# Kernel tuning notes

Measured on AMD Instinct MI355X. Metric: run time of the kernel, lower is better.

## Reference

```python
import jax, jax.numpy as jnp
import numpy as np

B, L, D = 32, 300, 256          # batch, seq (fixed 300 in module), emb_size
N = B * L                       # hypergraph nodes
NI, E, NNZ, U = 100000, 4000, 100000, 38312
LAYERS, HEADS, AH = 2, 4, 4     # conv layers, conv heads, fusing-attn heads
DU = D // 2                     # user embedding dim
DF = D + DU                     # fused dim (emb + emb//2)


def _pe_table():
    # pe[0] row is zeros (module indexes pe[0..L-1] where row 0 of buffer is zero)
    pos = jnp.arange(L, dtype=jnp.float32)[:, None]
    div = jnp.exp(jnp.arange(0, D, 2, dtype=jnp.float32) * (-np.log(10000.0) / D))
    pe = jnp.zeros((L + 1, D), jnp.float32)
    pe = pe.at[1:, 0::2].set(jnp.sin(pos * div))
    pe = pe.at[1:, 1::2].set(jnp.cos(pos * div))
    return pe[:L]  # [L, D]


def _hconv(x, W, b, node_idx, edge_idx):
    # Multi-head hypergraph conv: D^{-1} H B^{-1} H^T X Theta, heads concat back to D
    xt = (x @ W).reshape(N, HEADS, D // HEADS)
    ones = jnp.ones((NNZ,), x.dtype)
    deg_e = jnp.clip(jax.ops.segment_sum(ones, edge_idx, num_segments=E), 1.0)
    deg_n = jnp.clip(jax.ops.segment_sum(ones, node_idx, num_segments=N), 1.0)
    e = jax.ops.segment_sum(xt[node_idx], edge_idx, num_segments=E) / deg_e[:, None, None]
    o = jax.ops.segment_sum(e[edge_idx], node_idx, num_segments=N) / deg_n[:, None, None]
    return o.reshape(N, D) + b


def setup_inputs() -> dict:
    key = jax.random.key(0)
    ks = iter(jax.random.split(key, 40))
    s = 1.0 / 16.0  # stdv = 1/sqrt(emb_size) per reset_parameters
    u = lambda shape: jax.random.uniform(next(ks), shape, jnp.float32, -s, s)
    return {
        "input": jax.random.normal(next(ks), (B,), jnp.float32),
        "label": jax.random.normal(next(ks), (B,), jnp.float32),
        "text_table": jax.random.normal(next(ks), (NI, 384), jnp.float32) * 0.02,
        "img_table": jax.random.normal(next(ks), (NI, 2048), jnp.float32) * 0.02,
        "W1": u((384, D)), "b1": u((D,)),
        "W2": u((2048, D)), "b2": u((D,)),
        "user_table": u((U, DU)),
        "Wt": u((LAYERS, D, D)), "bt": u((LAYERS, D)),
        "Wi": u((LAYERS, D, D)), "bi": u((LAYERS, D)),
        "Wq": u((DF, DF)), "Wk": u((DF, DF)), "Wv": u((DF, DF)), "Wo": u((DF, DF)),
        "W3": u((2 * DF, DF)), "b3": u((DF,)),
        "Wd": u((DF, DF)), "bd": u((DF,)),
        "W4": u((DF, 1)), "b4": u((1,)),
        "related_items": jax.random.randint(next(ks), (N,), 0, NI),
        "uid": jax.random.randint(next(ks), (B,), 0, U),
        "hg_idx": jnp.stack([jax.random.randint(next(ks), (NNZ,), 0, N),
                             jax.random.randint(next(ks), (NNZ,), 0, E)]),
    }


def reference(input, label, text_table, img_table, W1, b1, W2, b2, user_table,
              Wt, bt, Wi, bi, Wq, Wk, Wv, Wo, W3, b3, Wd, bd, W4, b4,
              related_items, uid, hg_idx):
    ue = user_table[uid]                                    # [B, DU]
    pe = 0.002 * _pe_table()                                # added twice at *0.001 each
    te = (text_table[related_items] @ W1 + b1).reshape(B, L, D) + pe[None]
    ie = (img_table[related_items] @ W2 + b2).reshape(B, L, D) + pe[None]
    tg = te.reshape(N, D)
    ig = ie.reshape(N, D)
    node_idx, edge_idx = hg_idx[0], hg_idx[1]
    for l in range(LAYERS):  # fixed small layer count
        tg_new = _hconv(tg, Wt[l], bt[l], node_idx, edge_idx)
        ig = _hconv(ig, Wi[l], bi[l], node_idx, edge_idx)
        tg = tg_new
    text_user = jnp.concatenate([tg.reshape(B, L, D)[:, 0], ue], 1)  # [B, DF]
    img_user = jnp.concatenate([ig.reshape(B, L, D)[:, 0], ue], 1)   # [B, DF]
    fused = jnp.concatenate([text_user, img_user], -1) @ W3 + b3     # [B, DF]
    q = fused[:, None, :]                                   # [B, 1, DF]
    kv = jnp.stack([text_user, img_user], 1)                # [B, 2, DF]
    dh = DF // AH
    sp = lambda x: x.reshape(B, -1, AH, dh).transpose(0, 2, 1, 3)
    Qh, Kh, Vh = sp(q @ Wq), sp(kv @ Wk), sp(kv @ Wv)
    att = jax.nn.softmax(jnp.einsum('bhqd,bhkd->bhqk', Qh, Kh) / jnp.sqrt(jnp.float32(dh)), -1)
    o = jnp.einsum('bhqk,bhkd->bhqd', att, Vh).transpose(0, 2, 1, 3).reshape(B, 1, DF) @ Wo + q
    out = jax.nn.relu(o[:, 0, :] @ Wd + bd)                 # dense + ReLU
    return out @ W4 + b4                                    # [B, 1]
```

## Files before the change

kernel.cpp:

```cpp
#include <hip/hip_runtime.h>

typedef unsigned short u16;
typedef unsigned int u32;
typedef __bf16 bf16x8 __attribute__((ext_vector_type(8)));
typedef float f32x4 __attribute__((ext_vector_type(4)));

constexpr int Bn = 32, Ln = 300, Dn = 256;
constexpr int Nn = Bn * Ln;
constexpr int En = 4000, NNZn = 100000;
constexpr int DUn = 128, DFn = 384;
constexpr int PK = 512;
constexpr long NPl = (long)Nn * PK;
constexpr long EPl = (long)En * PK;
constexpr int PMAX = 1536;

constexpr int SEG_WPROD = 0;
constexpr int SEG_GIMG = SEG_WPROD + 512;
constexpr int SEG_W2T  = SEG_GIMG + 9600;
constexpr int SEG_GTXT = SEG_W2T + 2048;
constexpr int SEG_W1T  = SEG_GTXT + 2400;
constexpr int SEG_PE   = SEG_W1T + 384;
constexpr int SEG_CNT  = SEG_PE + 300;
constexpr int SEG_END  = SEG_CNT + 391;

__device__ __forceinline__ u16 f2bf(float f) {
    union { float f; u32 u; } x{f};
    u32 u = x.u;
    u32 r = (u + 0x7FFFu + ((u >> 16) & 1u)) >> 16;
    return (u16)r;
}
__device__ __forceinline__ float bf2f(u16 s) {
    union { u32 u; float f; } x{(u32)s << 16};
    return x.f;
}

__global__ __launch_bounds__(256) void prep_all(
    float* __restrict__ pe_tab,
    const float* __restrict__ W1, u16* __restrict__ W1t,
    const float* __restrict__ W2, u16* __restrict__ W2t,
    const float* __restrict__ Wt, const float* __restrict__ bt,
    const float* __restrict__ Wi, const float* __restrict__ bi,
    u16* __restrict__ W12t, float* __restrict__ bias12, float* __restrict__ bias2w,
    const int* __restrict__ node_idx, const int* __restrict__ edge_idx,
    int* __restrict__ cnt_e, int* __restrict__ cnt_n,
    const float* __restrict__ text_table, const float* __restrict__ img_table,
    const int* __restrict__ rel, u16* __restrict__ Atx, u16* __restrict__ Aim) {
    int bid = blockIdx.x;
    int t = threadIdx.x;
    if (bid < SEG_GIMG) {
        int idx = bid * 256 + t;
        int m = idx >> 16;
        int k = (idx >> 8) & 255;
        int n = idx & 255;
        const float* W0 = m ? Wi : Wt;
        const float* Wl1 = W0 + 65536;
        const float* b0 = m ? bi : bt;
        float acc = 0.f;
        for (int j = 0; j < 256; j++) acc += W0[k * 256 + j] * Wl1[j * 256 + n];
        W12t[((size_t)m << 16) + k * 256 + n] = f2bf(acc);
        if (k == 0) {
            float ba = 0.f;
            for (int j = 0; j < 256; j++) ba += b0[j] * Wl1[j * 256 + n];
            bias12[m * 256 + n] = ba + b0[256 + n];
            bias2w[m * 256 + n] = b0[256 + n];
        }
        return;
    }
    if (bid < SEG_W2T) {
        int r = bid - SEG_GIMG;
        const float4* s4 = (const float4*)(img_table + (size_t)rel[r] * 2048);
        u16* drow = Aim + (size_t)r * 2048;
#pragma unroll
        for (int i = 0; i < 2; i++) {
            int e = i * 256 + t;
            float4 v = s4[e];
            u16 o[4] = {f2bf(v.x), f2bf(v.y), f2bf(v.z), f2bf(v.w)};
            *(uint2*)&drow[e * 4] = *(uint2*)o;
        }
        return;
    }
    if (bid < SEG_GTXT) {
        int idx = (bid - SEG_W2T) * 256 + t;
        int k = idx >> 8, n = idx & 255;
        W2t[(size_t)n * 2048 + k] = f2bf(W2[idx]);
        return;
    }
    if (bid < SEG_W1T) {
        int base = (bid - SEG_GTXT) * 4;
#pragma unroll
        for (int i0 = 0; i0 < 2; i0++) {
            int i = i0 * 256 + t;
            if (i < 384) {
                int rr = i / 96, c4 = i % 96;
                int r = base + rr;
                const float4* s4 = (const float4*)(text_table + (size_t)rel[r] * 384);
                float4 v = s4[c4];
                u16 o[4] = {f2bf(v.x), f2bf(v.y), f2bf(v.z), f2bf(v.w)};
                *(uint2*)&Atx[(size_t)r * 384 + c4 * 4] = *(uint2*)o;
            }
        }
        return;
    }
    if (bid < SEG_PE) {
        int idx = (bid - SEG_W1T) * 256 + t;
        int k = idx >> 8, n = idx & 255;
        W1t[(size_t)n * 384 + k] = f2bf(W1[idx]);
        return;
    }
    if (bid < SEG_CNT) {
        int idx = (bid - SEG_PE) * 256 + t;
        int l = idx / Dn, c = idx % Dn;
        float v = 0.f;
        if (l > 0) {
            int j2 = c >> 1;
            float div = expf(-0.07195578415606394f * (float)j2);
            float ang = (float)(l - 1) * div;
            v = 0.002f * ((c & 1) ? cosf(ang) : sinf(ang));
        }
        pe_tab[idx] = v;
        return;
    }
    {
        int k = (bid - SEG_CNT) * 256 + t;
        if (k < NNZn) {
            atomicAdd(&cnt_e[edge_idx[k]], 1);
            atomicAdd(&cnt_n[node_idx[k]], 1);
        }
    }
}

__global__ void offs_kernel(const int* __restrict__ cnt_e, const int* __restrict__ cnt_n,
                            int* __restrict__ off_e, int* __restrict__ off_n,
                            float* __restrict__ invE, float* __restrict__ invN,
                            int* __restrict__ cursors) {
    int i = blockIdx.x * 256 + threadIdx.x;
    if (i < En) {
        int c = cnt_e[i];
        off_e[i] = atomicAdd(&cursors[0], c);
        invE[i] = 1.f / fmaxf((float)c, 1.f);
    }
    if (i < Nn) {
        int c = cnt_n[i];
        off_n[i] = atomicAdd(&cursors[1], c);
        invN[i] = 1.f / fmaxf((float)c, 1.f);
    }
}

__global__ void fill_csr(const int* __restrict__ node_idx, const int* __restrict__ edge_idx,
                         const int* __restrict__ off_e, const int* __restrict__ off_n,
                         int* __restrict__ cur_e, int* __restrict__ cur_n,
                         int* __restrict__ memb_e, int* __restrict__ memb_n, int nnz) {
    int k = blockIdx.x * blockDim.x + threadIdx.x;
    if (k < nnz) {
        int n = node_idx[k], ed = edge_idx[k];
        int pe = atomicAdd(&cur_e[ed], 1);
        memb_e[off_e[ed] + pe] = n;
        int pn = atomicAdd(&cur_n[n], 1);
        memb_n[off_n[n] + pn] = ed;
    }
}

#define LOFF(row, kc) (((row) << 6) + ((((kc) ^ ((row) & 7))) << 3))

__global__ __launch_bounds__(256) void gemm_proj(
    const u16* __restrict__ Atx, const u16* __restrict__ Aim,
    const u16* __restrict__ W1t, const u16* __restrict__ W2t,
    const float* __restrict__ b1, const float* __restrict__ b2,
    const float* __restrict__ pe_tab, u16* __restrict__ xg) {
    __shared__ u16 As[64 * 64];
    __shared__ u16 Bs[256 * 64];
    const int tid = threadIdx.x;
    const int lane = tid & 63;
    const int wv = tid >> 6;
    const int yy = blockIdx.y;
    const int z = (yy < 150) ? 1 : 0;
    const int m0 = ((yy < 150) ? yy : yy - 150) * 64;
    const int K = z ? 2048 : 384;
    const u16* A = z ? Aim : Atx;
    const u16* Bt = z ? W2t : W1t;
    const float* bias = z ? b2 : b1;
    const int coloff = z ? 256 : 0;

    const int srow = tid >> 3;
    const int skc = tid & 7;
    const u16* ap0 = A + (size_t)(m0 + srow) * K + skc * 8;
    const u16* ap1 = A + (size_t)(m0 + srow + 32) * K + skc * 8;
    const u16* bp = Bt + (size_t)srow * K + skc * 8;

    f32x4 acc[4][4] = {};
    uint4 rA0, rA1, rB[8];

    rA0 = *(const uint4*)(ap0);
    rA1 = *(const uint4*)(ap1);
#pragma unroll
    for (int it = 0; it < 8; it++) rB[it] = *(const uint4*)(bp + (size_t)(it * 32) * K);

    for (int k0 = 0; k0 < K; k0 += 64) {
        *(uint4*)&As[LOFF(srow, skc)] = rA0;
        *(uint4*)&As[LOFF(srow + 32, skc)] = rA1;
#pragma unroll
        for (int it = 0; it < 8; it++) *(uint4*)&Bs[LOFF(it * 32 + srow, skc)] = rB[it];
        __syncthreads();
        int kn = k0 + 64;
        if (kn < K) {
            rA0 = *(const uint4*)(ap0 + kn);
            rA1 = *(const uint4*)(ap1 + kn);
#pragma unroll
            for (int it = 0; it < 8; it++)
                rB[it] = *(const uint4*)(bp + (size_t)(it * 32) * K + kn);
        }
#pragma unroll
        for (int ks = 0; ks < 2; ks++) {
            int kc = ks * 4 + (lane >> 4);
            bf16x8 a[4], b[4];
#pragma unroll
            for (int mf = 0; mf < 4; mf++) a[mf] = *(bf16x8*)&As[LOFF(mf * 16 + (lane & 15), kc)];
#pragma unroll
            for (int nf = 0; nf < 4; nf++)
                b[nf] = *(bf16x8*)&Bs[LOFF(wv * 64 + nf * 16 + (lane & 15), kc)];
#pragma unroll
            for (int mf = 0; mf < 4; mf++)
#pragma unroll
                for (int nf = 0; nf < 4; nf++)
                    acc[mf][nf] = __builtin_amdgcn_mfma_f32_16x16x32_bf16(a[mf], b[nf], acc[mf][nf], 0, 0, 0);
        }
        __syncthreads();
    }

#pragma unroll
    for (int mf = 0; mf < 4; mf++) {
#pragma unroll
        for (int nf = 0; nf < 4; nf++) {
#pragma unroll
            for (int r = 0; r < 4; r++) {
                int row = m0 + mf * 16 + (lane >> 4) * 4 + r;
                int col = wv * 64 + nf * 16 + (lane & 15);
                float v = acc[mf][nf][r] + bias[col] + pe_tab[(row % Ln) * Dn + col];
                xg[(size_t)row * PK + coloff + col] = f2bf(v);
            }
        }
    }
}

__global__ __launch_bounds__(256) void agg_kernel(
    const u16* __restrict__ src, u16* __restrict__ dst,
    const int* __restrict__ memb, const int* __restrict__ off,
    const int* __restrict__ cnt, const float* __restrict__ inv, int nrows) {
    int row = blockIdx.x * 4 + (threadIdx.x >> 6);
    int lane = threadIdx.x & 63;
    if (row >= nrows) return;
    int s = off[row], tot = cnt[row];
    float acc[8] = {};
    const u16* base = src + (size_t)lane * 8;
    for (int cb = 0; cb < tot; cb += 64) {
        int m = min(64, tot - cb);
        int my = (lane < m) ? memb[s + cb + lane] : 0;
        for (int j = 0; j < m; j++) {
            int r = __builtin_amdgcn_readfirstlane(__shfl(my, j));
            uint4 v = *(const uint4*)(base + (size_t)r * PK);
            u16 h[8];
            *(uint4*)h = v;
#pragma unroll
            for (int q = 0; q < 8; q++) acc[q] += bf2f(h[q]);
        }
    }
    float sc = inv[row];
    u16 o[8];
#pragma unroll
    for (int j = 0; j < 8; j++) o[j] = f2bf(acc[j] * sc);
    *(uint4*)(dst + (size_t)row * PK + lane * 8) = *(uint4*)o;
}

__global__ __launch_bounds__(384) void tail_all(
    const u16* __restrict__ zg, const u16* __restrict__ W12t,
    const float* __restrict__ bias12, const float* __restrict__ bias2w,
    const int* __restrict__ off_e, const int* __restrict__ cnt_e, const int* __restrict__ memb_e,
    const int* __restrict__ off_n, const int* __restrict__ cnt_n, const int* __restrict__ memb_n,
    const float* __restrict__ invE, const float* __restrict__ invN,
    const float* __restrict__ ut, const int* __restrict__ uid,
    const float* __restrict__ W3, const float* __restrict__ b3,
    const float* __restrict__ Wq, const float* __restrict__ Wk,
    const float* __restrict__ Wv, const float* __restrict__ Wo,
    const float* __restrict__ Wd, const float* __restrict__ bd,
    const float* __restrict__ W4, const float* __restrict__ b4,
    float* __restrict__ out) {
    __shared__ float zrow[PK];
    __shared__ float kv0[DFn], kv1[DFn], Fv[DFn], qv[DFn];
    __shared__ float K0[DFn], K1[DFn], V0[DFn], V1[DFn], ov[DFn], o2[DFn];
    __shared__ int plist[PMAX];
    __shared__ float pw[PMAX];
    __shared__ float sarr[8], wgt[8], red[6];
    __shared__ int pcount;

    int b = blockIdx.x, t = threadIdx.x;
    int r = b * Ln;
    int ns = off_n[r], ne = cnt_n[r];

    if (t < 64) {
        int e = (t < ne) ? memb_n[ns + t] : 0;
        int es = (t < ne) ? off_e[e] : 0;
        int em = (t < ne) ? cnt_e[e] : 0;
        float w = (t < ne) ? invE[e] : 0.f;
        int pos = em;
#pragma unroll
        for (int o = 1; o < 64; o <<= 1) {
            int x = __shfl_up(pos, o);
            if (t >= o) pos += x;
        }
        int total = __shfl(pos, 63);
        pos -= em;
        for (int j = 0; j < em; j++) {
            if (pos + j < PMAX) {
                plist[pos + j] = memb_e[es + j];
                pw[pos + j] = w;
            }
        }
        if (t == 0) pcount = min(total, PMAX);
    }
    __syncthreads();
    int P = pcount;

    if (t < 256) {
        float za0 = 0.f, za1 = 0.f;
#pragma unroll 4
        for (int i = 0; i < P; i++) {
            int n = plist[i];
            float w = pw[i];
            u32 v = *(const u32*)&zg[(size_t)n * PK + 2 * t];
            za0 += bf2f((u16)(v & 0xffff)) * w;
            za1 += bf2f((u16)(v >> 16)) * w;
        }
        float sN = invN[r];
        zrow[2 * t] = za0 * sN;
        zrow[2 * t + 1] = za1 * sN;
    }
    __syncthreads();

    for (int c = t; c < 512; c += 384) {
        int m = c >> 8, cc = c & 255;
        float acc;
        if (ne == 0) {
            acc = bias2w[c];
        } else {
            acc = bias12[c];
            const u16* wp = W12t + ((size_t)m << 16) + cc;
            for (int k = 0; k < 256; k++) acc += zrow[m * 256 + k] * bf2f(wp[(size_t)k * 256]);
        }
        if (m == 0) kv0[cc] = acc;
        else kv1[cc] = acc;
    }
    if (t < 128) {
        float u = ut[(size_t)uid[b] * DUn + t];
        kv0[256 + t] = u;
        kv1[256 + t] = u;
    }
    __syncthreads();

    {
        int c = t;
        float acc = b3[c];
        for (int k = 0; k < DFn; k++) acc += kv0[k] * W3[(size_t)k * DFn + c];
        for (int k = 0; k < DFn; k++) acc += kv1[k] * W3[(size_t)(DFn + k) * DFn + c];
        Fv[c] = acc;
    }
    __syncthreads();

    {
        int c = t;
        float aq = 0.f, ak0 = 0.f, ak1 = 0.f, av0 = 0.f, av1 = 0.f;
        for (int k = 0; k < DFn; k++) {
            float wk = Wk[(size_t)k * DFn + c];
            float wvv = Wv[(size_t)k * DFn + c];
            aq += Fv[k] * Wq[(size_t)k * DFn + c];
            ak0 += kv0[k] * wk;
            ak1 += kv1[k] * wk;
            av0 += kv0[k] * wvv;
            av1 += kv1[k] * wvv;
        }
        qv[c] = aq;
        K0[c] = ak0;
        K1[c] = ak1;
        V0[c] = av0;
        V1[c] = av1;
    }
    __syncthreads();

    if (t < 256) {
        int g = t >> 5, l = t & 31;
        int h = g >> 1, wch = g & 1;
        const float* Kp = (wch ? K1 : K0) + h * 96;
        const float* qp = qv + h * 96;
        float p = 0.f;
        for (int d = l; d < 96; d += 32) p += qp[d] * Kp[d];
#pragma unroll
        for (int o = 16; o; o >>= 1) p += __shfl_down(p, o, 32);
        if (l == 0) sarr[g] = p * 0.10206207261596575f;
    }
    __syncthreads();
    if (t < 4) {
        float s0 = sarr[2 * t], s1 = sarr[2 * t + 1];
        float m = fmaxf(s0, s1);
        float e0 = expf(s0 - m), e1 = expf(s1 - m);
        float inv = 1.f / (e0 + e1);
        wgt[2 * t] = e0 * inv;
        wgt[2 * t + 1] = e1 * inv;
    }
    __syncthreads();
    {
        int c = t;
        int h = c / 96;
        ov[c] = wgt[2 * h] * V0[c] + wgt[2 * h + 1] * V1[c];
    }
    __syncthreads();
    {
        int c = t;
        float acc = Fv[c];
        for (int k = 0; k < DFn; k++) acc += ov[k] * Wo[(size_t)k * DFn + c];
        o2[c] = acc;
    }
    __syncthreads();
    {
        int c = t;
        float acc = bd[c];
        for (int k = 0; k < DFn; k++) acc += o2[k] * Wd[(size_t)k * DFn + c];
        qv[c] = fmaxf(acc, 0.f);
    }
    __syncthreads();
    float p2 = qv[t] * W4[t];
#pragma unroll
    for (int o = 32; o; o >>= 1) p2 += __shfl_down(p2, o);
    if ((t & 63) == 0) red[t >> 6] = p2;
    __syncthreads();
    if (t == 0)
        out[b] = red[0] + red[1] + red[2] + red[3] + red[4] + red[5] + b4[0];
}

extern "C" void kernel_launch(void* const* d_in, const int* in_sizes, int n_in,
                              void* d_out, int out_size, void* d_ws, size_t ws_size,
                              hipStream_t stream) {
    const float* text_table = (const float*)d_in[2];
    const float* img_table  = (const float*)d_in[3];
    const float* W1 = (const float*)d_in[4];
    const float* b1 = (const float*)d_in[5];
    const float* W2 = (const float*)d_in[6];
    const float* b2 = (const float*)d_in[7];
    const float* user_table = (const float*)d_in[8];
    const float* Wt = (const float*)d_in[9];
    const float* bt = (const float*)d_in[10];
    const float* Wi = (const float*)d_in[11];
    const float* bi = (const float*)d_in[12];
    const float* Wq = (const float*)d_in[13];
    const float* Wk = (const float*)d_in[14];
    const float* Wv = (const float*)d_in[15];
    const float* Wo = (const float*)d_in[16];
    const float* W3 = (const float*)d_in[17];
    const float* b3 = (const float*)d_in[18];
    const float* Wd = (const float*)d_in[19];
    const float* bd = (const float*)d_in[20];
    const float* W4 = (const float*)d_in[21];
    const float* b4 = (const float*)d_in[22];
    const int* rel = (const int*)d_in[23];
    const int* uid = (const int*)d_in[24];
    const int* hg  = (const int*)d_in[25];
    const int* node_idx = hg;
    const int* edge_idx = hg + NNZn;

    u16* xg  = (u16*)d_ws;
    u16* eP  = xg + NPl;
    u16* zg  = eP + EPl;
    u16* Atx = zg + NPl;
    u16* Aim = Atx + (size_t)Nn * 384;
    u16* W1t = Aim + (size_t)Nn * 2048;
    u16* W2t = W1t + 98304;
    u16* W12t = W2t + 524288;
    float* invE   = (float*)(W12t + 131072);
    float* invN   = invE + En;
    float* pe_tab = invN + Nn;
    float* bias12 = pe_tab + Ln * Dn;
    float* bias2w = bias12 + 512;
    int* cnt_e  = (int*)(bias2w + 512);
    int* cnt_n  = cnt_e + En;
    int* cur_e  = cnt_n + Nn;
    int* cur_n  = cur_e + En;
    int* cursors = cur_n + Nn;
    int* off_e  = cursors + 2;
    int* off_n  = off_e + En;
    int* memb_e = off_n + Nn;
    int* memb_n = memb_e + NNZn;
    float* outp = (float*)d_out;

    hipMemsetAsync(cnt_e, 0, (size_t)(2 * (En + Nn) + 2) * sizeof(int), stream);
    prep_all<<<SEG_END, 256, 0, stream>>>(pe_tab, W1, W1t, W2, W2t, Wt, bt, Wi, bi,
                                          W12t, bias12, bias2w, node_idx, edge_idx,
                                          cnt_e, cnt_n, text_table, img_table, rel,
                                          Atx, Aim);
    offs_kernel<<<(Nn + 255) / 256, 256, 0, stream>>>(cnt_e, cnt_n, off_e, off_n, invE, invN, cursors);
    fill_csr<<<(NNZn + 255) / 256, 256, 0, stream>>>(node_idx, edge_idx, off_e, off_n,
                                                     cur_e, cur_n, memb_e, memb_n, NNZn);
    dim3 grdP(1, 300, 1);
    gemm_proj<<<grdP, 256, 0, stream>>>(Atx, Aim, W1t, W2t, b1, b2, pe_tab, xg);
    agg_kernel<<<En / 4, 256, 0, stream>>>(xg, eP, memb_e, off_e, cnt_e, invE, En);
    agg_kernel<<<Nn / 4, 256, 0, stream>>>(eP, zg, memb_n, off_n, cnt_n, invN, Nn);
    tail_all<<<Bn, 384, 0, stream>>>(zg, W12t, bias12, bias2w, off_e, cnt_e, memb_e,
                                     off_n, cnt_n, memb_n, invE, invN, user_table, uid,
                                     W3, b3, Wq, Wk, Wv, Wo, Wd, bd, W4, b4, outp);
}
```

Before: 321.5 us.

## Pre-transpose tail weights to bf16, widen tail block, fuse offsets into GEMM

The tail weights (Wq, Wk, Wv, Wo, Wd, W3 and the combined layer weight) are converted once in the prep kernel to bf16 in column-major order. Each tail thread can then read its output column's weights contiguously with 16-byte loads, instead of strided fp32 loads. The tail kernel grows to 768 threads, splitting the node aggregation three ways and pairing the K/V projections across thread halves. The separate offsets kernel is folded into extra blocks of the projection GEMM launch to save one launch. The tail math now uses bf16 weights, which lowers precision, and the prep kernel does more work.

```diff
diff --git a/kernel.cpp b/kernel.cpp
--- a/kernel.cpp
+++ b/kernel.cpp
@@ -15,13 +15,15 @@
 constexpr int PMAX = 1536;
 
 constexpr int SEG_WPROD = 0;
-constexpr int SEG_GIMG = SEG_WPROD + 512;
-constexpr int SEG_W2T  = SEG_GIMG + 9600;
-constexpr int SEG_GTXT = SEG_W2T + 2048;
-constexpr int SEG_W1T  = SEG_GTXT + 2400;
-constexpr int SEG_PE   = SEG_W1T + 384;
-constexpr int SEG_CNT  = SEG_PE + 300;
-constexpr int SEG_END  = SEG_CNT + 391;
+constexpr int SEG_GIMG  = SEG_WPROD + 512;
+constexpr int SEG_W2T   = SEG_GIMG + 9600;
+constexpr int SEG_GTXT  = SEG_W2T + 2048;
+constexpr int SEG_W1T   = SEG_GTXT + 2400;
+constexpr int SEG_WTAIL = SEG_W1T + 384;
+constexpr int SEG_W3C   = SEG_WTAIL + 2880;
+constexpr int SEG_PE    = SEG_W3C + 1152;
+constexpr int SEG_CNT   = SEG_PE + 300;
+constexpr int SEG_END   = SEG_CNT + 391;
 
 __device__ __forceinline__ u16 f2bf(float f) {
     union { float f; u32 u; } x{f};
@@ -32,6 +34,16 @@
 __device__ __forceinline__ float bf2f(u16 s) {
     union { u32 u; float f; } x{(u32)s << 16};
     return x.f;
+}
+
+__device__ __forceinline__ float dot8(const u16* __restrict__ w, const float* __restrict__ x) {
+    uint4 v = *(const uint4*)w;
+    u16 h[8];
+    *(uint4*)h = v;
+    float s = 0.f;
+#pragma unroll
+    for (int j = 0; j < 8; j++) s += x[j] * bf2f(h[j]);
+    return s;
 }
 
 __global__ __launch_bounds__(256) void prep_all(
@@ -40,11 +52,15 @@
     const float* __restrict__ W2, u16* __restrict__ W2t,
     const float* __restrict__ Wt, const float* __restrict__ bt,
     const float* __restrict__ Wi, const float* __restrict__ bi,
-    u16* __restrict__ W12t, float* __restrict__ bias12, float* __restrict__ bias2w,
+    u16* __restrict__ W12c, float* __restrict__ bias12, float* __restrict__ bias2w,
     const int* __restrict__ node_idx, const int* __restrict__ edge_idx,
     int* __restrict__ cnt_e, int* __restrict__ cnt_n,
     const float* __restrict__ text_table, const float* __restrict__ img_table,
-    const int* __restrict__ rel, u16* __restrict__ Atx, u16* __restrict__ Aim) {
+    const int* __restrict__ rel, u16* __restrict__ Atx, u16* __restrict__ Aim,
+    const float* __restrict__ Wq, const float* __restrict__ Wk,
+    const float* __restrict__ Wv, const float* __restrict__ Wo,
+    const float* __restrict__ Wd, u16* __restrict__ Wtail,
+    const float* __restrict__ W3, u16* __restrict__ W3c) {
     int bid = blockIdx.x;
     int t = threadIdx.x;
     if (bid < SEG_GIMG) {
@@ -56,8 +72,9 @@
         const float* Wl1 = W0 + 65536;
         const float* b0 = m ? bi : bt;
         float acc = 0.f;
+#pragma unroll 8
         for (int j = 0; j < 256; j++) acc += W0[k * 256 + j] * Wl1[j * 256 + n];
-        W12t[((size_t)m << 16) + k * 256 + n] = f2bf(acc);
+        W12c[((size_t)m << 16) + n * 256 + k] = f2bf(acc);
         if (k == 0) {
             float ba = 0.f;
             for (int j = 0; j < 256; j++) ba += b0[j] * Wl1[j * 256 + n];
@@ -101,10 +118,25 @@
         }
         return;
     }
-    if (bid < SEG_PE) {
+    if (bid < SEG_WTAIL) {
         int idx = (bid - SEG_W1T) * 256 + t;
         int k = idx >> 8, n = idx & 255;
         W1t[(size_t)n * 384 + k] = f2bf(W1[idx]);
+        return;
+    }
+    if (bid < SEG_W3C) {
+        int idx = (bid - SEG_WTAIL) * 256 + t;
+        int w = idx / 147456;
+        int rem = idx - w * 147456;
+        int k = rem / 384, c = rem - k * 384;
+        const float* S = (w == 0) ? Wq : (w == 1) ? Wk : (w == 2) ? Wv : (w == 3) ? Wo : Wd;
+        Wtail[(size_t)w * 147456 + (size_t)c * 384 + k] = f2bf(S[rem]);
+        return;
+    }
+    if (bid < SEG_PE) {
+        int idx = (bid - SEG_W3C) * 256 + t;
+        int k = idx / 384, c = idx - k * 384;
+        W3c[(size_t)c * 768 + k] = f2bf(W3[idx]);
         return;
     }
     if (bid < SEG_CNT) {
@@ -126,23 +158,6 @@
             atomicAdd(&cnt_e[edge_idx[k]], 1);
             atomicAdd(&cnt_n[node_idx[k]], 1);
         }
-    }
-}
-
-__global__ void offs_kernel(const int* __restrict__ cnt_e, const int* __restrict__ cnt_n,
-                            int* __restrict__ off_e, int* __restrict__ off_n,
-                            float* __restrict__ invE, float* __restrict__ invN,
-                            int* __restrict__ cursors) {
-    int i = blockIdx.x * 256 + threadIdx.x;
-    if (i < En) {
-        int c = cnt_e[i];
-        off_e[i] = atomicAdd(&cursors[0], c);
-        invE[i] = 1.f / fmaxf((float)c, 1.f);
-    }
-    if (i < Nn) {
-        int c = cnt_n[i];
-        off_n[i] = atomicAdd(&cursors[1], c);
-        invN[i] = 1.f / fmaxf((float)c, 1.f);
     }
 }
 
@@ -162,17 +177,34 @@
 
 #define LOFF(row, kc) (((row) << 6) + ((((kc) ^ ((row) & 7))) << 3))
 
-__global__ __launch_bounds__(256) void gemm_proj(
+__global__ __launch_bounds__(256) void gemm_offs(
     const u16* __restrict__ Atx, const u16* __restrict__ Aim,
     const u16* __restrict__ W1t, const u16* __restrict__ W2t,
     const float* __restrict__ b1, const float* __restrict__ b2,
-    const float* __restrict__ pe_tab, u16* __restrict__ xg) {
+    const float* __restrict__ pe_tab, u16* __restrict__ xg,
+    const int* __restrict__ cnt_e, const int* __restrict__ cnt_n,
+    int* __restrict__ off_e, int* __restrict__ off_n,
+    float* __restrict__ invE, float* __restrict__ invN, int* __restrict__ cursors) {
     __shared__ u16 As[64 * 64];
     __shared__ u16 Bs[256 * 64];
     const int tid = threadIdx.x;
+    const int yy = blockIdx.y;
+    if (yy >= 300) {
+        int i = (yy - 300) * 256 + tid;
+        if (i < En) {
+            int c = cnt_e[i];
+            off_e[i] = atomicAdd(&cursors[0], c);
+            invE[i] = 1.f / fmaxf((float)c, 1.f);
+        }
+        if (i < Nn) {
+            int c = cnt_n[i];
+            off_n[i] = atomicAdd(&cursors[1], c);
+            invN[i] = 1.f / fmaxf((float)c, 1.f);
+        }
+        return;
+    }
     const int lane = tid & 63;
     const int wv = tid >> 6;
-    const int yy = blockIdx.y;
     const int z = (yy < 150) ? 1 : 0;
     const int m0 = ((yy < 150) ? yy : yy - 150) * 64;
     const int K = z ? 2048 : 384;
@@ -271,26 +303,32 @@
     *(uint4*)(dst + (size_t)row * PK + lane * 8) = *(uint4*)o;
 }
 
-__global__ __launch_bounds__(384) void tail_all(
-    const u16* __restrict__ zg, const u16* __restrict__ W12t,
+__global__ __launch_bounds__(768) void tail_all(
+    const u16* __restrict__ zg, const u16* __restrict__ W12c,
     const float* __restrict__ bias12, const float* __restrict__ bias2w,
     const int* __restrict__ off_e, const int* __restrict__ cnt_e, const int* __restrict__ memb_e,
     const int* __restrict__ off_n, const int* __restrict__ cnt_n, const int* __restrict__ memb_n,
     const float* __restrict__ invE, const float* __restrict__ invN,
     const float* __restrict__ ut, const int* __restrict__ uid,
-    const float* __restrict__ W3, const float* __restrict__ b3,
-    const float* __restrict__ Wq, const float* __restrict__ Wk,
-    const float* __restrict__ Wv, const float* __restrict__ Wo,
-    const float* __restrict__ Wd, const float* __restrict__ bd,
+    const u16* __restrict__ W3c, const float* __restrict__ b3,
+    const u16* __restrict__ Wtail, const float* __restrict__ bd,
     const float* __restrict__ W4, const float* __restrict__ b4,
     float* __restrict__ out) {
     __shared__ float zrow[PK];
-    __shared__ float kv0[DFn], kv1[DFn], Fv[DFn], qv[DFn];
+    __shared__ float psum[3][PK];
+    __shared__ float kvc[768];
+    __shared__ float Fv[DFn], qv[DFn];
     __shared__ float K0[DFn], K1[DFn], V0[DFn], V1[DFn], ov[DFn], o2[DFn];
     __shared__ int plist[PMAX];
     __shared__ float pw[PMAX];
-    __shared__ float sarr[8], wgt[8], red[6];
+    __shared__ float sarr[8], wgt[8], red[12];
     __shared__ int pcount;
+
+    const u16* Wqc = Wtail;
+    const u16* Wkc = Wtail + 147456;
+    const u16* Wvc = Wtail + 294912;
+    const u16* Woc = Wtail + 442368;
+    const u16* Wdc = Wtail + 589824;
 
     int b = blockIdx.x, t = threadIdx.x;
     int r = b * Ln;
@@ -320,68 +358,94 @@
     __syncthreads();
     int P = pcount;
 
-    if (t < 256) {
+    {
+        int g = t >> 8;
+        int c2 = t & 255;
         float za0 = 0.f, za1 = 0.f;
-#pragma unroll 4
-        for (int i = 0; i < P; i++) {
+        for (int i = g; i < P; i += 3) {
             int n = plist[i];
             float w = pw[i];
-            u32 v = *(const u32*)&zg[(size_t)n * PK + 2 * t];
+            u32 v = *(const u32*)&zg[(size_t)n * PK + 2 * c2];
             za0 += bf2f((u16)(v & 0xffff)) * w;
             za1 += bf2f((u16)(v >> 16)) * w;
         }
-        float sN = invN[r];
-        zrow[2 * t] = za0 * sN;
-        zrow[2 * t + 1] = za1 * sN;
-    }
-    __syncthreads();
-
-    for (int c = t; c < 512; c += 384) {
-        int m = c >> 8, cc = c & 255;
+        psum[g][2 * c2] = za0;
+        psum[g][2 * c2 + 1] = za1;
+    }
+    __syncthreads();
+    if (t < PK) {
+        zrow[t] = (psum[0][t] + psum[1][t] + psum[2][t]) * invN[r];
+    }
+    __syncthreads();
+
+    if (t < 512) {
+        int m = t >> 8, cc = t & 255;
         float acc;
         if (ne == 0) {
-            acc = bias2w[c];
+            acc = bias2w[t];
         } else {
-            acc = bias12[c];
-            const u16* wp = W12t + ((size_t)m << 16) + cc;
-            for (int k = 0; k < 256; k++) acc += zrow[m * 256 + k] * bf2f(wp[(size_t)k * 256]);
-        }
-        if (m == 0) kv0[cc] = acc;
-        else kv1[cc] = acc;
-    }
-    if (t < 128) {
-        float u = ut[(size_t)uid[b] * DUn + t];
-        kv0[256 + t] = u;
-        kv1[256 + t] = u;
-    }
-    __syncthreads();
-
-    {
-        int c = t;
-        float acc = b3[c];
-        for (int k = 0; k < DFn; k++) acc += kv0[k] * W3[(size_t)k * DFn + c];
-        for (int k = 0; k < DFn; k++) acc += kv1[k] * W3[(size_t)(DFn + k) * DFn + c];
-        Fv[c] = acc;
-    }
-    __syncthreads();
-
-    {
-        int c = t;
-        float aq = 0.f, ak0 = 0.f, ak1 = 0.f, av0 = 0.f, av1 = 0.f;
-        for (int k = 0; k < DFn; k++) {
-            float wk = Wk[(size_t)k * DFn + c];
-            float wvv = Wv[(size_t)k * DFn + c];
-            aq += Fv[k] * Wq[(size_t)k * DFn + c];
-            ak0 += kv0[k] * wk;
-            ak1 += kv1[k] * wk;
-            av0 += kv0[k] * wvv;
-            av1 += kv1[k] * wvv;
-        }
-        qv[c] = aq;
-        K0[c] = ak0;
-        K1[c] = ak1;
-        V0[c] = av0;
-        V1[c] = av1;
+            acc = bias12[t];
+            const u16* wp = W12c + ((size_t)m << 16) + cc * 256;
+            const float* zp = zrow + m * 256;
+#pragma unroll 4
+            for (int k0 = 0; k0 < 256; k0 += 8) acc += dot8(wp + k0, zp + k0);
+        }
+        kvc[m * 384 + cc] = acc;
+    } else if (t < 640) {
+        int i = t - 512;
+        float u = ut[(size_t)uid[b] * DUn + i];
+        kvc[256 + i] = u;
+        kvc[640 + i] = u;
+    }
+    __syncthreads();
+
+    if (t < 384) {
+        float acc = b3[t];
+        const u16* wp = W3c + (size_t)t * 768;
+#pragma unroll 4
+        for (int k0 = 0; k0 < 768; k0 += 8) acc += dot8(wp + k0, kvc + k0);
+        Fv[t] = acc;
+    }
+    __syncthreads();
+
+    if (t < 384) {
+        float acc = 0.f;
+        const u16* wp = Wqc + (size_t)t * 384;
+#pragma unroll 4
+        for (int k0 = 0; k0 < 384; k0 += 8) acc += dot8(wp + k0, Fv + k0);
+        qv[t] = acc;
+    } else {
+        int c = t - 384;
+        float acc = 0.f;
+        const u16* wp = Wkc + (size_t)c * 384;
+#pragma unroll 4
+        for (int k0 = 0; k0 < 384; k0 += 8) acc += dot8(wp + k0, kvc + k0);
+        K0[c] = acc;
+    }
+    __syncthreads();
+
+    if (t < 384) {
+        float acc = 0.f;
+        const u16* wp = Wkc + (size_t)t * 384;
+#pragma unroll 4
+        for (int k0 = 0; k0 < 384; k0 += 8) acc += dot8(wp + k0, kvc + 384 + k0);
+        K1[t] = acc;
+    } else {
+        int c = t - 384;
+        float acc = 0.f;
+        const u16* wp = Wvc + (size_t)c * 384;
+#pragma unroll 4
+        for (int k0 = 0; k0 < 384; k0 += 8) acc += dot8(wp + k0, kvc + k0);
+        V0[c] = acc;
+    }
+    __syncthreads();
+
+    if (t < 384) {
+        float acc = 0.f;
+        const u16* wp = Wvc + (size_t)t * 384;
+#pragma unroll 4
+        for (int k0 = 0; k0 < 384; k0 += 8) acc += dot8(wp + k0, kvc + 384 + k0);
+        V1[t] = acc;
     }
     __syncthreads();
 
@@ -406,33 +470,38 @@
         wgt[2 * t + 1] = e1 * inv;
     }
     __syncthreads();
-    {
-        int c = t;
-        int h = c / 96;
-        ov[c] = wgt[2 * h] * V0[c] + wgt[2 * h + 1] * V1[c];
-    }
-    __syncthreads();
-    {
-        int c = t;
-        float acc = Fv[c];
-        for (int k = 0; k < DFn; k++) acc += ov[k] * Wo[(size_t)k * DFn + c];
-        o2[c] = acc;
-    }
-    __syncthreads();
-    {
-        int c = t;
-        float acc = bd[c];
-        for (int k = 0; k < DFn; k++) acc += o2[k] * Wd[(size_t)k * DFn + c];
-        qv[c] = fmaxf(acc, 0.f);
-    }
-    __syncthreads();
-    float p2 = qv[t] * W4[t];
+    if (t < 384) {
+        int h = t / 96;
+        ov[t] = wgt[2 * h] * V0[t] + wgt[2 * h + 1] * V1[t];
+    }
+    __syncthreads();
+    if (t < 384) {
+        float acc = Fv[t];
+        const u16* wp = Woc + (size_t)t * 384;
+#pragma unroll 4
+        for (int k0 = 0; k0 < 384; k0 += 8) acc += dot8(wp + k0, ov + k0);
+        o2[t] = acc;
+    }
+    __syncthreads();
+    if (t < 384) {
+        float acc = bd[t];
+        const u16* wp = Wdc + (size_t)t * 384;
+#pragma unroll 4
+        for (int k0 = 0; k0 < 384; k0 += 8) acc += dot8(wp + k0, o2 + k0);
+        qv[t] = fmaxf(acc, 0.f);
+    }
+    __syncthreads();
+    float p2 = (t < 384) ? qv[t] * W4[t] : 0.f;
 #pragma unroll
     for (int o = 32; o; o >>= 1) p2 += __shfl_down(p2, o);
     if ((t & 63) == 0) red[t >> 6] = p2;
     __syncthreads();
-    if (t == 0)
-        out[b] = red[0] + red[1] + red[2] + red[3] + red[4] + red[5] + b4[0];
+    if (t == 0) {
+        float s = b4[0];
+#pragma unroll
+        for (int i = 0; i < 12; i++) s += red[i];
+        out[b] = s;
+    }
 }
 
 extern "C" void kernel_launch(void* const* d_in, const int* in_sizes, int n_in,
@@ -472,8 +541,10 @@
     u16* Aim = Atx + (size_t)Nn * 384;
     u16* W1t = Aim + (size_t)Nn * 2048;
     u16* W2t = W1t + 98304;
-    u16* W12t = W2t + 524288;
-    float* invE   = (float*)(W12t + 131072);
+    u16* W12c = W2t + 524288;
+    u16* Wtail = W12c + 131072;
+    u16* W3c = Wtail + 737280;
+    float* invE   = (float*)(W3c + 294912);
     float* invN   = invE + En;
     float* pe_tab = invN + Nn;
     float* bias12 = pe_tab + Ln * Dn;
@@ -491,17 +562,17 @@
 
     hipMemsetAsync(cnt_e, 0, (size_t)(2 * (En + Nn) + 2) * sizeof(int), stream);
     prep_all<<<SEG_END, 256, 0, stream>>>(pe_tab, W1, W1t, W2, W2t, Wt, bt, Wi, bi,
-                                          W12t, bias12, bias2w, node_idx, edge_idx,
+                                          W12c, bias12, bias2w, node_idx, edge_idx,
                                           cnt_e, cnt_n, text_table, img_table, rel,
-                                          Atx, Aim);
-    offs_kernel<<<(Nn + 255) / 256, 256, 0, stream>>>(cnt_e, cnt_n, off_e, off_n, invE, invN, cursors);
+                                          Atx, Aim, Wq, Wk, Wv, Wo, Wd, Wtail, W3, W3c);
+    dim3 grdP(1, 338, 1);
+    gemm_offs<<<grdP, 256, 0, stream>>>(Atx, Aim, W1t, W2t, b1, b2, pe_tab, xg,
+                                        cnt_e, cnt_n, off_e, off_n, invE, invN, cursors);
     fill_csr<<<(NNZn + 255) / 256, 256, 0, stream>>>(node_idx, edge_idx, off_e, off_n,
                                                      cur_e, cur_n, memb_e, memb_n, NNZn);
-    dim3 grdP(1, 300, 1);
-    gemm_proj<<<grdP, 256, 0, stream>>>(Atx, Aim, W1t, W2t, b1, b2, pe_tab, xg);
     agg_kernel<<<En / 4, 256, 0, stream>>>(xg, eP, memb_e, off_e, cnt_e, invE, En);
     agg_kernel<<<Nn / 4, 256, 0, stream>>>(eP, zg, memb_n, off_n, cnt_n, invN, Nn);
-    tail_all<<<Bn, 384, 0, stream>>>(zg, W12t, bias12, bias2w, off_e, cnt_e, memb_e,
+    tail_all<<<Bn, 768, 0, stream>>>(zg, W12c, bias12, bias2w, off_e, cnt_e, memb_e,
                                      off_n, cnt_n, memb_n, invE, invN, user_table, uid,
-                                     W3, b3, Wq, Wk, Wv, Wo, Wd, bd, W4, b4, outp);
-}
+                                     W3c, b3, Wtail, bd, W4, b4, outp);
+}
```

Measured after the change: 329.5 us. 2.5% more time.
